# Optimization experiments

Measured on AMD Instinct MI355X. Metric: run time of the kernel, lower is better.

Reference implementation:

```python
import jax, jax.numpy as jnp
import numpy as np

ALPHA = 0.2  # LeakyReLU negative slope


def setup_inputs() -> dict:
    key = jax.random.key(0)
    k0, k1, k2, k3 = jax.random.split(key, 4)
    N, H, W, T, V = 16, 32, 32, 16, 64
    h = jax.random.normal(k0, (N, H, W, T, V), jnp.float32)
    conv_w = jax.random.normal(k1, (3, 3, T, T), jnp.float32) * 0.05  # HWIO
    conv_b = jnp.zeros((T,), jnp.float32)
    a = jax.random.normal(k2, (2 * H * W, 1), jnp.float32) * 0.03  # ~xavier scale
    B = jax.random.uniform(k3, (V, V), jnp.float32)
    return {"h": h, "conv_w": conv_w, "conv_b": conv_b, "a": a, "B": B}


def reference(h, conv_w, conv_b, a, B):
    N, H, W, T, V = h.shape
    hv = jnp.transpose(h, (0, 4, 1, 2, 3))  # (N,V,H,W,T)

    # ConvMapping: 3x3 SAME conv over spatial dims with T as channels
    x = hv.reshape(N * V, H, W, T)
    y = jax.lax.conv_general_dilated(
        x, conv_w, (1, 1), 'SAME',
        dimension_numbers=('NHWC', 'HWIO', 'NHWC')) + conv_b
    Wh = y.reshape(N, V, H, W, T)

    # Attention logits. Original builds concat([Wh_i, Wh_j], dim=W) with trailing
    # layout (H, 2W, T) then row-major views it as (T, 2*H*W). We reproduce that
    # exact reinterpretation, but exploit additivity over i/j so the O(V^2)
    # pair tensor is never materialized.
    HW2 = 2 * H * W
    zeros = jnp.zeros_like(Wh)
    Cl = jnp.concatenate([Wh, zeros], axis=3).reshape(N, V, T, HW2)
    Cr = jnp.concatenate([zeros, Wh], axis=3).reshape(N, V, T, HW2)
    av = a[:, 0]
    Ei = jnp.einsum('bvtk,k->bvt', Cl, av)
    Ej = jnp.einsum('bvtk,k->bvt', Cr, av)
    e = jax.nn.leaky_relu(Ei[:, :, None, :] + Ej[:, None, :, :], ALPHA)  # (N,V,V,T)
    att = jax.nn.softmax(e, axis=-1)  # softmax over time dim, as in original

    # Symmetric-normalized adjacency: D^-1/2 (B + I, min-max scaled) D^-1/2
    adj = B + jnp.eye(V, dtype=B.dtype)
    adj = (adj - adj.min()) / (adj.max() - adj.min())
    d12 = 1.0 / jnp.sqrt(jnp.sum(adj, axis=1))
    adj_norm = adj * d12[:, None] * d12[None, :]

    # Aggregation: h_prime[b,p,t,i] = sum_j Wh[b,j,p,t] * att[b,i,j,t]
    # (replaces the original V^2 python loop + diag_embed matmuls)
    Whf = Wh.reshape(N, V, H * W, T)
    hp = jnp.einsum('bjpt,bijt->bpti', Whf, att)  # (N,HW,T,V)
    out = jnp.einsum('bpti,iv->bptv', hp, adj_norm)
    return jax.nn.elu(out.reshape(N, H, W, T, V))
```

## Files before the change

kernel.cpp:

```cpp
#include <hip/hip_runtime.h>
#include <hip/hip_bf16.h>
#include <math.h>

#define ALPHA_ 0.2f
#define N_ 16
#define H_ 32
#define W_ 32
#define T_ 16
#define V_ 64
#define P_ (H_*W_)

typedef __bf16 bf16x8 __attribute__((ext_vector_type(8)));
typedef float  f32x4  __attribute__((ext_vector_type(4)));

static __device__ inline bf16x8 zero8() {
    bf16x8 z;
    #pragma unroll
    for (int i = 0; i < 8; ++i) z[i] = (__bf16)0.f;
    return z;
}

static __device__ inline unsigned short bf16bits(float f) {
    __hip_bfloat16 b = __float2bfloat16(f);
    return *reinterpret_cast<unsigned short*>(&b);
}

static __device__ inline __bf16 tobf(float f) {
    unsigned short u = bf16bits(f);
    return *reinterpret_cast<__bf16*>(&u);
}

__global__ __launch_bounds__(256, 4) void tr2_k(const float* __restrict__ X,
                                                __hip_bfloat16* __restrict__ Xt,
                                                const float* __restrict__ CW,
                                                const float* __restrict__ Bm,
                                                __hip_bfloat16* __restrict__ Bfrag,
                                                float* __restrict__ adjn) {
    int bid = blockIdx.x;
    int tid = threadIdx.x;

    if (bid == N_*34*4) {
        __shared__ float sd[64];
        float row[64];
        int lane = tid;
        if (tid < 64) {
            int t = lane & 15, kg = lane >> 4;
            #pragma unroll
            for (int dw = 0; dw < 3; ++dw) {
                #pragma unroll
                for (int pr = 0; pr < 2; ++pr) {
                    __hip_bfloat16* dst = Bfrag + ((size_t)((dw*2+pr)*64 + lane))*8;
                    #pragma unroll
                    for (int i = 0; i < 8; ++i) {
                        int ti = (kg & 1)*8 + i;
                        float val;
                        if (pr == 0) { int dh = kg >> 1; val = CW[((dh*3+dw)*16+ti)*16 + t]; }
                        else          val = (kg < 2) ? CW[((2*3+dw)*16+ti)*16 + t] : 0.f;
                        dst[i] = __float2bfloat16(val);
                    }
                }
            }
            int i = lane;
            float mn = 1e30f, mx = -1e30f;
            #pragma unroll
            for (int v = 0; v < 64; ++v) {
                float x = Bm[i*64 + v] + (v == i ? 1.f : 0.f);
                row[v] = x;
                mn = fminf(mn, x);
                mx = fmaxf(mx, x);
            }
            #pragma unroll
            for (int off = 32; off > 0; off >>= 1) {
                mn = fminf(mn, __shfl_xor(mn, off));
                mx = fmaxf(mx, __shfl_xor(mx, off));
            }
            float inv = 1.f / (mx - mn);
            float rs = 0.f;
            #pragma unroll
            for (int v = 0; v < 64; ++v) {
                row[v] = (row[v] - mn) * inv;
                rs += row[v];
            }
            sd[i] = rsqrtf(rs);
        }
        __syncthreads();
        if (tid < 64) {
            float d = sd[tid];
            #pragma unroll
            for (int v = 0; v < 64; ++v) adjn[tid*64 + v] = row[v] * d * sd[v];
        }
        return;
    }

    int b   = bid / 136;
    int r   = bid % 136;
    int hp  = r >> 2;
    int wq  = r & 3;

    __hip_bfloat16* dst = Xt + (((size_t)(b*34 + hp)*W_ + wq*8) * V_) * T_;

    if (hp == 0 || hp == 33) {
        uint4 z = {0u,0u,0u,0u};
        uint4* d = (uint4*)dst;
        #pragma unroll
        for (int k = 0; k < 4; ++k) d[tid + 256*k] = z;
        return;
    }
    int h = hp - 1;

    __shared__ __align__(16) unsigned sx[4096];

    int vq  = tid & 15;
    int tp4 = (tid >> 4) & 3;
    int w4  = tid >> 6;
    const float* Xb = X + (((size_t)(b*H_ + h)*W_ + wq*8) * T_) * V_ + vq*4;

    f32x4 xr[2][2][2];
    #pragma unroll
    for (int iw = 0; iw < 2; ++iw) {
        int wl = iw*4 + w4;
        #pragma unroll
        for (int th = 0; th < 2; ++th) {
            #pragma unroll
            for (int tk = 0; tk < 2; ++tk) {
                int ti = (th*4 + tp4)*2 + tk;
                xr[iw][th][tk] = *(const f32x4*)(Xb + ((size_t)wl*T_ + ti)*V_);
            }
        }
    }
    #pragma unroll
    for (int iw = 0; iw < 2; ++iw) {
        int wl = iw*4 + w4;
        #pragma unroll
        for (int th = 0; th < 2; ++th) {
            int tp = th*4 + tp4;
            uint4 pk;
            unsigned* pw = (unsigned*)&pk;
            #pragma unroll
            for (int k2 = 0; k2 < 4; ++k2)
                pw[k2] = (unsigned)bf16bits(xr[iw][th][0][k2])
                       | ((unsigned)bf16bits(xr[iw][th][1][k2]) << 16);
            *(uint4*)&sx[(wl*8 + tp)*64 + (vq ^ tp4)*4] = pk;
        }
    }
    __syncthreads();

    #pragma unroll
    for (int k = 0; k < 4; ++k) {
        int c   = tid + 256*k;
        int wl  = c >> 7;
        int vv  = (c >> 1) & 63;
        int thf = c & 1;
        uint4 o;
        unsigned* ow = (unsigned*)&o;
        #pragma unroll
        for (int q = 0; q < 4; ++q)
            ow[q] = sx[(wl*8 + thf*4 + q)*64 + ((vv >> 2) ^ q)*4 + (vv & 3)];
        *(uint4*)(dst + ((size_t)wl*V_ + vv)*T_ + thf*8) = o;
    }
}

__global__ __launch_bounds__(256, 4) void conv_k(const __hip_bfloat16* __restrict__ Xt,
                                                 const __hip_bfloat16* __restrict__ Bfrag,
                                                 const float* __restrict__ CB,
                                                 const float* __restrict__ av,
                                                 __hip_bfloat16* __restrict__ Whb,
                                                 float* __restrict__ Eihi,
                                                 float* __restrict__ Eihj) {
    __shared__ float sEi[4][16], sEj[4][16];

    int orig = blockIdx.x;
    int bi   = (orig & 7) * 256 + (orig >> 3);
    int b    = bi >> 7;
    int rem  = bi & 127;
    int h    = rem >> 2;
    int vg   = rem & 3, vb = vg * 16;

    int tid = threadIdx.x, lane = tid & 63, wc = tid >> 6;
    int lm = lane & 15, kg = lane >> 4;

    bf16x8 Bf01[3], Bf2[3];
    #pragma unroll
    for (int dw = 0; dw < 3; ++dw) {
        Bf01[dw] = *(const bf16x8*)(Bfrag + (size_t)((dw*2+0)*64 + lane)*8);
        Bf2 [dw] = *(const bf16x8*)(Bfrag + (size_t)((dw*2+1)*64 + lane)*8);
    }
    float cb = CB[lm];
    f32x4 acc[8];
    #pragma unroll
    for (int wi = 0; wi < 8; ++wi) acc[wi] = (f32x4){cb, cb, cb, cb};

    const __hip_bfloat16* base01 =
        Xt + ((size_t)((b*34 + h + (kg>>1))*W_)*V_ + vb + lm)*T_ + (kg&1)*8;
    const __hip_bfloat16* base2  =
        Xt + ((size_t)((b*34 + h + 2)*W_)*V_ + vb + lm)*T_ + (kg&1)*8;

    #pragma unroll
    for (int u = 0; u < 10; ++u) {
        int wxu = wc*8 + u - 1;
        bf16x8 f01 = zero8(), f2 = zero8();
        if ((unsigned)wxu < (unsigned)W_) {
            f01 = *(const bf16x8*)(base01 + (size_t)wxu*(V_*T_));
            f2  = *(const bf16x8*)(base2  + (size_t)wxu*(V_*T_));
        }
        #pragma unroll
        for (int dw = 0; dw < 3; ++dw) {
            int wi = u - dw;
            if (wi >= 0 && wi < 8) {
                acc[wi] = __builtin_amdgcn_mfma_f32_16x16x32_bf16(f01, Bf01[dw], acc[wi], 0, 0, 0);
                acc[wi] = __builtin_amdgcn_mfma_f32_16x16x32_bf16(f2,  Bf2 [dw], acc[wi], 0, 0, 0);
            }
        }
    }

    float si[4] = {0.f,0.f,0.f,0.f}, sj[4] = {0.f,0.f,0.f,0.f};
    {
        const float* avb = av + (h & 1)*1024 + wc*8*16 + lm;
        #pragma unroll
        for (int wi = 0; wi < 8; ++wi) {
            float ai = avb[wi*16];
            float aj = avb[wi*16 + 512];
            #pragma unroll
            for (int r = 0; r < 4; ++r) {
                si[r] += acc[wi][r] * ai;
                sj[r] += acc[wi][r] * aj;
            }
        }
        #pragma unroll
        for (int off = 1; off < 16; off <<= 1) {
            #pragma unroll
            for (int r = 0; r < 4; ++r) {
                si[r] += __shfl_xor(si[r], off);
                sj[r] += __shfl_xor(sj[r], off);
            }
        }
    }
    if (lm == 0) {
        #pragma unroll
        for (int r = 0; r < 4; ++r) {
            sEi[wc][kg*4 + r] = si[r];
            sEj[wc][kg*4 + r] = sj[r];
        }
    }

    #pragma unroll
    for (int wi = 0; wi < 8; ++wi) {
        int p = h*W_ + wc*8 + wi;
        unsigned short u0 = bf16bits(acc[wi][0]);
        unsigned short u1 = bf16bits(acc[wi][1]);
        unsigned short u2 = bf16bits(acc[wi][2]);
        unsigned short u3 = bf16bits(acc[wi][3]);
        uint2 pk;
        pk.x = (unsigned)u0 | ((unsigned)u1 << 16);
        pk.y = (unsigned)u2 | ((unsigned)u3 << 16);
        *(uint2*)(Whb + ((size_t)(b*T_ + lm)*P_ + p)*V_ + vb + kg*4) = pk;
    }

    __syncthreads();
    if (tid < 16) {
        float a = sEi[0][tid] + sEi[1][tid] + sEi[2][tid] + sEi[3][tid];
        float c = sEj[0][tid] + sEj[1][tid] + sEj[2][tid] + sEj[3][tid];
        Eihi[((size_t)b*H_ + h)*V_ + vb + tid] = a;
        Eihj[((size_t)b*H_ + h)*V_ + vb + tid] = c;
    }
}

__global__ __launch_bounds__(256, 4) void att_m_k(const float* __restrict__ Eihi,
                                                  const float* __restrict__ Eihj,
                                                  const float* __restrict__ adjn,
                                                  __hip_bfloat16* __restrict__ Mt) {
    int b = blockIdx.x >> 6;
    int j = blockIdx.x & 63;
    int tid = threadIdx.x;
    __shared__ float s_att[64][16];
    __shared__ float sadj[4096];

    #pragma unroll
    for (int k = 0; k < 16; ++k) sadj[tid + 256*k] = adjn[tid + 256*k];

    if (tid < 64) {
        int i = tid;
        const float* ebi = Eihi + (size_t)b*H_*V_;
        const float* ebj = Eihj + (size_t)b*H_*V_;
        float ev[16];
        float mxe = -1e30f;
        #pragma unroll
        for (int t = 0; t < 16; ++t) {
            float x = ebi[(2*t)*V_ + i] + ebi[(2*t+1)*V_ + i]
                    + ebj[(2*t)*V_ + j] + ebj[(2*t+1)*V_ + j];
            x = (x >= 0.f) ? x : ALPHA_ * x;
            ev[t] = x;
            mxe = fmaxf(mxe, x);
        }
        float s = 0.f;
        #pragma unroll
        for (int t = 0; t < 16; ++t) {
            ev[t] = __expf(ev[t] - mxe);
            s += ev[t];
        }
        float invs = 1.f / s;
        #pragma unroll
        for (int t = 0; t < 16; ++t) s_att[i][t] = ev[t] * invs;
    }
    __syncthreads();

    int v = tid & 63, tq = tid >> 6;
    float acc[4] = {0.f, 0.f, 0.f, 0.f};
    for (int i = 0; i < 64; ++i) {
        float an = sadj[i*64 + v];
        #pragma unroll
        for (int u = 0; u < 4; ++u) acc[u] += s_att[i][tq*4 + u] * an;
    }
    #pragma unroll
    for (int u = 0; u < 4; ++u) {
        int t = tq*4 + u;
        Mt[(((size_t)b*T_ + t)*V_ + v)*V_ + j] = __float2bfloat16(acc[u]);
    }
}

__global__ __launch_bounds__(256, 6) void out_k(const __hip_bfloat16* __restrict__ Whb,
                                                const __hip_bfloat16* __restrict__ Mt,
                                                float* __restrict__ out) {
    int orig = blockIdx.x;
    int bi   = (orig & 7) * 256 + (orig >> 3);
    int pc = bi & 7;
    int t  = (bi >> 3) & 15;
    int b  = bi >> 7;

    int tid  = threadIdx.x;
    int lane = tid & 63;
    int wid  = tid >> 6;
    int lm   = lane & 15;
    int lk   = lane >> 4;

    const __hip_bfloat16* Ab = Whb + ((size_t)(b*T_ + t)*P_ + pc*128) * V_;
    const __hip_bfloat16* Bb = Mt  + (size_t)(b*T_ + t) * (V_*V_);

    f32x4 acc[2][4];
    #pragma unroll
    for (int pt = 0; pt < 2; ++pt)
        #pragma unroll
        for (int vt = 0; vt < 4; ++vt) acc[pt][vt] = (f32x4){0.f,0.f,0.f,0.f};

    #pragma unroll
    for (int kf = 0; kf < 2; ++kf) {
        int ko = kf*32 + lk*8;
        bf16x8 a0 = *(const bf16x8*)(Ab + ((size_t)((wid*2+0)*16 + lm))*V_ + ko);
        bf16x8 a1 = *(const bf16x8*)(Ab + ((size_t)((wid*2+1)*16 + lm))*V_ + ko);
        #pragma unroll
        for (int vt = 0; vt < 4; ++vt) {
            bf16x8 bf = *(const bf16x8*)(Bb + ((size_t)(vt*16 + lm))*V_ + ko);
            acc[0][vt] = __builtin_amdgcn_mfma_f32_16x16x32_bf16(a0, bf, acc[0][vt], 0, 0, 0);
            acc[1][vt] = __builtin_amdgcn_mfma_f32_16x16x32_bf16(a1, bf, acc[1][vt], 0, 0, 0);
        }
    }

    #pragma unroll
    for (int pt = 0; pt < 2; ++pt) {
        #pragma unroll
        for (int vt = 0; vt < 4; ++vt) {
            #pragma unroll
            for (int r = 0; r < 4; ++r) {
                int p  = pc*128 + (wid*2 + pt)*16 + lk*4 + r;
                int vv = vt*16 + lm;
                float x = acc[pt][vt][r];
                x = (x > 0.f) ? x : (__expf(x) - 1.f);
                out[((size_t)(b*P_ + p)*T_ + t)*V_ + vv] = x;
            }
        }
    }
}

extern "C" void kernel_launch(void* const* d_in, const int* in_sizes, int n_in,
                              void* d_out, int out_size, void* d_ws, size_t ws_size,
                              hipStream_t stream) {
    const float* X  = (const float*)d_in[0];
    const float* CW = (const float*)d_in[1];
    const float* CB = (const float*)d_in[2];
    const float* av = (const float*)d_in[3];
    const float* Bm = (const float*)d_in[4];
    float* outp = (float*)d_out;

    __hip_bfloat16* Whb = (__hip_bfloat16*)d_ws;
    __hip_bfloat16* Mt  = Whb + (size_t)N_*T_*P_*V_;
    float* Eihi = (float*)(Mt + (size_t)N_*T_*V_*V_);
    float* Eihj = Eihi + (size_t)N_*H_*V_;
    float* adjn = Eihj + (size_t)N_*H_*V_;
    __hip_bfloat16* Bfrag = (__hip_bfloat16*)(adjn + V_*V_);

    __hip_bfloat16* Xt = (__hip_bfloat16*)d_out;

    tr2_k  <<<N_*34*4 + 1, 256, 0, stream>>>(X, Xt, CW, Bm, Bfrag, adjn);
    conv_k <<<2048,        256, 0, stream>>>(Xt, Bfrag, CB, av, Whb, Eihi, Eihj);
    att_m_k<<<N_*V_,       256, 0, stream>>>(Eihi, Eihj, adjn, Mt);
    out_k  <<<N_*T_*8,     256, 0, stream>>>(Whb, Mt, outp);
}
```

Baseline: 76.87 us.

## Pad staged input along width and hoist all conv loads ahead of MFMAs

The transposed bf16 staging buffer now carries zero padding on both width edges, so the conv kernel no longer needs per-tap bounds checks and zero fills. The conv kernel issues all 20 fragment loads up front, then runs the MFMA chain, which gives the loads more overlap. Launch bounds drop from 4 to 3 waves per SIMD to make room for the extra registers, at the cost of some occupancy. The transpose kernel writes the extra padding columns, which adds a little memory traffic.

```diff
diff --git a/kernel.cpp b/kernel.cpp
--- a/kernel.cpp
+++ b/kernel.cpp
@@ -10,24 +10,16 @@
 #define V_ 64
 #define P_ (H_*W_)
 
+#define HP_ 34
+#define WP_ 34
+#define XROW_ (WP_*V_*T_)
+
 typedef __bf16 bf16x8 __attribute__((ext_vector_type(8)));
 typedef float  f32x4  __attribute__((ext_vector_type(4)));
-
-static __device__ inline bf16x8 zero8() {
-    bf16x8 z;
-    #pragma unroll
-    for (int i = 0; i < 8; ++i) z[i] = (__bf16)0.f;
-    return z;
-}
 
 static __device__ inline unsigned short bf16bits(float f) {
     __hip_bfloat16 b = __float2bfloat16(f);
     return *reinterpret_cast<unsigned short*>(&b);
-}
-
-static __device__ inline __bf16 tobf(float f) {
-    unsigned short u = bf16bits(f);
-    return *reinterpret_cast<__bf16*>(&u);
 }
 
 __global__ __launch_bounds__(256, 4) void tr2_k(const float* __restrict__ X,
@@ -97,7 +89,16 @@
     int hp  = r >> 2;
     int wq  = r & 3;
 
-    __hip_bfloat16* dst = Xt + (((size_t)(b*34 + hp)*W_ + wq*8) * V_) * T_;
+    __hip_bfloat16* rowbase = Xt + ((size_t)b*HP_ + hp) * XROW_;
+    __hip_bfloat16* dst = rowbase + (size_t)(wq*8 + 1) * (V_*T_);
+
+    if (wq == 0) {
+        uint4 z = {0u,0u,0u,0u};
+        if (tid < 128) ((uint4*)rowbase)[tid] = z;
+    } else if (wq == 3) {
+        uint4 z = {0u,0u,0u,0u};
+        if (tid < 128) ((uint4*)(rowbase + (size_t)33*(V_*T_)))[tid] = z;
+    }
 
     if (hp == 0 || hp == 33) {
         uint4 z = {0u,0u,0u,0u};
@@ -160,7 +161,7 @@
     }
 }
 
-__global__ __launch_bounds__(256, 4) void conv_k(const __hip_bfloat16* __restrict__ Xt,
+__global__ __launch_bounds__(256, 3) void conv_k(const __hip_bfloat16* __restrict__ Xt,
                                                  const __hip_bfloat16* __restrict__ Bfrag,
                                                  const float* __restrict__ CB,
                                                  const float* __restrict__ av,
@@ -191,24 +192,27 @@
     for (int wi = 0; wi < 8; ++wi) acc[wi] = (f32x4){cb, cb, cb, cb};
 
     const __hip_bfloat16* base01 =
-        Xt + ((size_t)((b*34 + h + (kg>>1))*W_)*V_ + vb + lm)*T_ + (kg&1)*8;
+        Xt + ((size_t)(b*HP_ + h + (kg>>1)))*XROW_
+           + (size_t)(wc*8)*(V_*T_) + (vb + lm)*T_ + (kg&1)*8;
     const __hip_bfloat16* base2  =
-        Xt + ((size_t)((b*34 + h + 2)*W_)*V_ + vb + lm)*T_ + (kg&1)*8;
-
+        Xt + ((size_t)(b*HP_ + h + 2))*XROW_
+           + (size_t)(wc*8)*(V_*T_) + (vb + lm)*T_ + (kg&1)*8;
+
+    bf16x8 f01[10], f2[10];
     #pragma unroll
     for (int u = 0; u < 10; ++u) {
-        int wxu = wc*8 + u - 1;
-        bf16x8 f01 = zero8(), f2 = zero8();
-        if ((unsigned)wxu < (unsigned)W_) {
-            f01 = *(const bf16x8*)(base01 + (size_t)wxu*(V_*T_));
-            f2  = *(const bf16x8*)(base2  + (size_t)wxu*(V_*T_));
-        }
+        f01[u] = *(const bf16x8*)(base01 + (size_t)u*(V_*T_));
+        f2 [u] = *(const bf16x8*)(base2  + (size_t)u*(V_*T_));
+    }
+
+    #pragma unroll
+    for (int u = 0; u < 10; ++u) {
         #pragma unroll
         for (int dw = 0; dw < 3; ++dw) {
             int wi = u - dw;
             if (wi >= 0 && wi < 8) {
-                acc[wi] = __builtin_amdgcn_mfma_f32_16x16x32_bf16(f01, Bf01[dw], acc[wi], 0, 0, 0);
-                acc[wi] = __builtin_amdgcn_mfma_f32_16x16x32_bf16(f2,  Bf2 [dw], acc[wi], 0, 0, 0);
+                acc[wi] = __builtin_amdgcn_mfma_f32_16x16x32_bf16(f01[u], Bf01[dw], acc[wi], 0, 0, 0);
+                acc[wi] = __builtin_amdgcn_mfma_f32_16x16x32_bf16(f2 [u], Bf2 [dw], acc[wi], 0, 0, 0);
             }
         }
     }
```

After: 77.25 us. Within noise of the previous version (+0.5%).
